# Optimization experiments

Hardware: AMD Instinct MI355X
Metric: run time of the kernel (lower is better)

The kernel has to match this reference:

```python
import jax, jax.numpy as jnp
import numpy as np

# Module constants (from init_kwargs / defaults)
OUT_SIZE = (4, 32, 32)      # (Z, X, Y) grid
REAL_SIZE = (3.0, 25.0, 25.0)
SCALE = 1.4
THRESHOLD = 0.5
D_ELEMS = np.array([0.74 * SCALE, 0.528 * SCALE], dtype=np.float32)  # per-element match/NMS radius (O, H)


def _transform(x):
    """(B, X, Y, Z, 4*E) -> coords (B, E, N, 3), conf (B, E, N); N = Z*X*Y."""
    B, X, Y, Z, L = x.shape
    E = L // 4
    v = x.reshape(B, X, Y, Z, E, 4).transpose(0, 4, 3, 1, 2, 5)   # (B,E,Z,X,Y,4)
    v = v[..., jnp.array([2, 0, 1, 3])]                            # reorder last dim
    Zs, Xs, Ys = OUT_SIZE
    ind = jnp.stack(jnp.meshgrid(jnp.arange(Zs), jnp.arange(Xs), jnp.arange(Ys), indexing='ij'),
                    axis=-1).astype(x.dtype)                       # (Z,X,Y,3) == torch nonzero of ones
    expand = jnp.array([r / o for o, r in zip(OUT_SIZE, REAL_SIZE)], dtype=x.dtype)
    coords = (v[..., :3] + ind) * expand
    conf = v[..., 3]
    N = Zs * Xs * Ys
    return coords.reshape(B, E, N, 3), conf.reshape(B, E, N)


def _sort_by_conf(coords, conf):
    order = jnp.argsort(-conf, axis=-1)
    coords = jnp.take_along_axis(coords, order[..., None], axis=2)
    conf = jnp.take_along_axis(conf, order, axis=-1)
    return coords, conf


def _nms(pts, valid, d):
    """Greedy sequential NMS on one (N,3) point set. Point b is suppressed if any
    still-selected earlier point a<b lies within distance d. Invalid points never suppress."""
    N = pts.shape[0]
    d2 = jnp.sum((pts[:, None, :] - pts[None, :, :]) ** 2, axis=-1)   # (N,N)
    ar = jnp.arange(N)
    M = (d2 < d * d) & valid[:, None] & valid[None, :] & (ar[:, None] < ar[None, :])

    def body(b, sel):
        return sel.at[b].set(~jnp.any(sel & M[:, b]))

    sel = jax.lax.fori_loop(0, N, body, jnp.ones((N,), bool))
    return sel & valid


def _match(P, T, keepP, keepT, d):
    """Greedy row-major bipartite matching: each pred (in order) grabs the first
    still-unmatched target within distance d. Returns (TP, FP, FN) masks."""
    N = P.shape[0]
    d2 = jnp.sum((P[:, None, :] - T[None, :, :]) ** 2, axis=-1)      # (N,N)
    D = (d2 < d * d) & keepP[:, None] & keepT[None, :]

    def body(a, carry):
        selP, selT = carry
        avail = D[a] & ~selT
        has = jnp.any(avail)
        j = jnp.argmax(avail)                    # first available target index
        selT = selT.at[j].set(selT[j] | has)
        selP = selP.at[a].set(has)
        return (selP, selT)

    selP, selT = jax.lax.fori_loop(0, N, body,
                                   (jnp.zeros((N,), bool), jnp.zeros((N,), bool)))
    return selP, keepP & ~selP, keepT & ~selT    # TP, FP, FN masks


def setup_inputs() -> dict:
    key = jax.random.key(0)
    k1, k2 = jax.random.split(key)
    B = 4
    predictions = jax.random.normal(k1, (B, 32, 32, 4, 8), dtype=jnp.float32)
    targets = jax.random.normal(k2, (B, 32, 32, 4, 8), dtype=jnp.float32)
    return {"predictions": predictions, "targets": targets}


def reference(predictions, targets):
    Pc, Pconf = _sort_by_conf(*_transform(predictions))   # (B,E,N,3), (B,E,N)
    Tc, Tconf = _sort_by_conf(*_transform(targets))
    validP = Pconf > THRESHOLD
    validT = Tconf > THRESHOLD
    d = jnp.asarray(D_ELEMS)                               # (E,)

    nms_be = jax.vmap(jax.vmap(_nms, in_axes=(0, 0, 0)), in_axes=(0, 0, None))
    keepP = nms_be(Pc, validP, d)                          # (B,E,N) bool
    keepT = nms_be(Tc, validT, d)

    match_be = jax.vmap(jax.vmap(_match, in_axes=(0, 0, 0, 0, 0)), in_axes=(0, 0, 0, 0, None))
    tp, fp, fn = match_be(Pc, Tc, keepP, keepT, d)         # (B,E,N) bool each

    # sorted real-space points, NMS-kept masks, and TP/FP/FN masks (fixed-shape
    # equivalents of the torch module's filtered P/T/TP/FP/FN lists)
    return Pc, Tc, keepP, keepT, tp, fp, fn
```

## Files before the change

kernel.cpp:

```cpp
#include <hip/hip_runtime.h>
#include <hip/hip_bf16.h>

#pragma clang fp contract(off)

#define NPTS 4096
#define BE   8
#define COORD_SZ (BE * NPTS * 3)
#define MASK_SZ  (BE * NPTS)
#define OFF_PC   0
#define OFF_TC   (COORD_SZ)
#define OFF_KP   (2 * COORD_SZ)
#define OFF_KT   (2 * COORD_SZ + MASK_SZ)
#define OFF_TP   (2 * COORD_SZ + 2 * MASK_SZ)
#define OFF_FP   (2 * COORD_SZ + 3 * MASK_SZ)
#define OFF_FN   (2 * COORD_SZ + 4 * MASK_SZ)

#define VCAP 1664
#define NW   26

#define WS_V_OFF     524288ull
#define WS_KEEP_OFF  524352ull
#define WS_PP_OFF    528448ull
#define WS_PT_OFF    6066240ull
#define WS_NEED      8835136ull

#define NBC 16

typedef unsigned long long u64;

__device__ __forceinline__ float get_dd(int e) {
    const float d0 = (float)(0.74 * 1.4);
    const float d1 = (float)(0.528 * 1.4);
    float d = (e == 0) ? d0 : d1;
    return d * d;
}

__global__ __launch_bounds__(1024)
void sort_kernel(const float* __restrict__ pred,
                 const float* __restrict__ targ,
                 float* __restrict__ out,
                 int* __restrict__ Vcnt) {
    __shared__ u64 bufA[NPTS], bufB[NPTS];
    __shared__ unsigned int hist[1024];
    __shared__ unsigned int offarr[1024];
    __shared__ int wsum[16];
    __shared__ int vtot;
    const int s = blockIdx.x;
    const int arr = s & 1, be = s >> 1;
    const int b = be >> 1, e = be & 1;
    const float* __restrict__ src = arr ? targ : pred;
    const int t = threadIdx.x;
    const int lane = t & 63, wv = t >> 6;

    if (t == 0) vtot = 0;
    for (int n = t; n < NPTS; n += 1024) {
        int z = n >> 10, r = n & 1023, x = r >> 5, y = r & 31;
        int base = (((b * 32 + x) * 32 + y) * 4 + z) * 8 + e * 4;
        float conf = src[base + 3];
        unsigned int bits = __float_as_uint(conf);
        unsigned int u = (bits & 0x80000000u) ? ~bits : (bits | 0x80000000u);
        bufA[n] = ((u64)(~u) << 32) | (unsigned int)n;
    }
    __syncthreads();

    const u64 lmask = (1ull << lane) - 1ull;
    for (int k = 0; k < 8; ++k) {
        u64* cur = (k & 1) ? bufB : bufA;
        u64* nxt = (k & 1) ? bufA : bufB;
        const int shift = 32 + (k << 2);
        hist[t] = 0u;
        __syncthreads();

        u64 item[4]; int dg[4]; int rnk[4];
        #pragma unroll
        for (int m = 0; m < 4; ++m) {
            u64 it = cur[m * 1024 + t];
            int d = (int)((it >> shift) & 15);
            u64 eq = ~0ull;
            #pragma unroll
            for (int bb = 0; bb < 4; ++bb) {
                u64 bal = __ballot((d >> bb) & 1);
                eq &= ((d >> bb) & 1) ? bal : ~bal;
            }
            int r = (int)__popcll(eq & lmask);
            if (r == 0) hist[d * 64 + m * 16 + wv] = (unsigned int)__popcll(eq);
            item[m] = it; dg[m] = d; rnk[m] = r;
        }
        __syncthreads();

        {
            int v = (int)hist[t];
            int inc = v;
            #pragma unroll
            for (int dd = 1; dd < 64; dd <<= 1) {
                int x2 = __shfl_up(inc, dd);
                if (lane >= dd) inc += x2;
            }
            if (lane == 63) wsum[wv] = inc;
            __syncthreads();
            if (t < 16) {
                int wtot = wsum[t]; int iv = wtot;
                #pragma unroll
                for (int dd = 1; dd < 16; dd <<= 1) {
                    int x2 = __shfl_up(iv, dd);
                    if (t >= dd) iv += x2;
                }
                wsum[t] = iv - wtot;
            }
            __syncthreads();
            offarr[t] = (unsigned int)(wsum[wv] + (inc - v));
        }
        __syncthreads();

        #pragma unroll
        for (int m = 0; m < 4; ++m) {
            int pos = (int)offarr[dg[m] * 64 + m * 16 + wv] + rnk[m];
            nxt[pos] = item[m];
        }
        __syncthreads();
    }

    int myv = 0;
    for (int p = t; p < NPTS; p += 1024) {
        u64 key = bufA[p];
        int n = (int)(key & 0xFFFFFFFFull);
        myv += ((unsigned int)(key >> 32) < 0x40FFFFFFu) ? 1 : 0;
        int z = n >> 10, rr = n & 1023, x = rr >> 5, y = rr & 31;
        int base = (((b * 32 + x) * 32 + y) * 4 + z) * 8 + e * 4;
        float r0 = src[base + 0], r1 = src[base + 1], r2 = src[base + 2];
        float c0 = (r2 + (float)z) * 0.75f;
        float c1 = (r0 + (float)x) * 0.78125f;
        float c2 = (r1 + (float)y) * 0.78125f;
        float* dst = out + (size_t)arr * COORD_SZ + ((size_t)be * NPTS + p) * 3;
        dst[0] = c0; dst[1] = c1; dst[2] = c2;
    }
    atomicAdd(&vtot, myv);
    __syncthreads();
    if (t == 0) Vcnt[s] = vtot;
}

__global__ __launch_bounds__(256)
void matrix_kernel(const float* __restrict__ out,
                   const int* __restrict__ Vcnt,
                   u64* __restrict__ ws64) {
    __shared__ float4 tcol[VCAP];
    __shared__ float rowc[64][3];
    const int bx = blockIdx.x;
    const int j = bx / 26, c = bx % 26;
    const int t = threadIdx.x;

    int sRow, sCol, e;
    u64* dstBase;
    if (j < 16) {
        sRow = j; sCol = j; e = (j >> 1) & 1;
        dstBase = ws64 + (WS_PP_OFF / 8) + (size_t)j * VCAP * NW;
    } else {
        int be = j - 16;
        sRow = be * 2 + 0; sCol = be * 2 + 1; e = be & 1;
        dstBase = ws64 + (WS_PT_OFF / 8) + (size_t)be * VCAP * NW;
    }
    int Vr = Vcnt[sRow]; if (Vr > VCAP) Vr = VCAP;
    int Vc = Vcnt[sCol]; if (Vc > VCAP) Vc = VCAP;
    const int rb = c * 64;
    if (rb >= Vr) return;
    const float dd = get_dd(e);

    const float* __restrict__ colc = out + (size_t)(sCol & 1) * COORD_SZ + (size_t)(sCol >> 1) * NPTS * 3;
    const float* __restrict__ rowp = out + (size_t)(sRow & 1) * COORD_SZ + (size_t)(sRow >> 1) * NPTS * 3;

    for (int idx = t; idx < Vc * 3; idx += 256) {
        float v = colc[idx];
        int p = idx / 3, k = idx % 3;
        ((float*)&tcol[p])[k] = v;
    }
    for (int idx = t; idx < 192; idx += 256) {
        int i = idx / 3, k = idx % 3;
        if (rb + i < Vr) rowc[i][k] = rowp[(rb + i) * 3 + k];
    }
    __syncthreads();

    const int NWc = (Vc + 63) >> 6;
    const int wlimit = (j < 16) ? (c + 1) : NWc;
    const int i = t & 63;
    const bool rowOK = (rb + i) < Vr;
    if (rowOK) {
        float ax = rowc[i][0], ay = rowc[i][1], az = rowc[i][2];
        for (int w = t >> 6; w < wlimit; w += 4) {
            int jbase = w << 6;
            int jmax = Vc - jbase; if (jmax > 64) jmax = 64;
            u64 m = 0ull;
            for (int jj = 0; jj < jmax; ++jj) {
                float4 tc = tcol[jbase + jj];
                float dx = ax - tc.x, dy = ay - tc.y, dz = az - tc.z;
                float d2 = dx * dx + dy * dy + dz * dz;
                m |= (d2 < dd) ? (1ull << jj) : 0ull;
            }
            dstBase[(size_t)w * VCAP + (rb + i)] = m;
        }
    }
}

__global__ __launch_bounds__(1024)
void nms_rounds_kernel(float* __restrict__ out,
                       const int* __restrict__ Vcnt,
                       u64* __restrict__ ws64) {
    __shared__ unsigned short nbr[VCAP][NBC];
    __shared__ unsigned short nbrcnt[VCAP];
    __shared__ unsigned char stbuf[VCAP];
    __shared__ int remaining;
    volatile unsigned char* st = stbuf;
    const int s = blockIdx.x;
    const int arr = s & 1, be = s >> 1;
    const int t = threadIdx.x;
    int V = Vcnt[s]; if (V > VCAP) V = VCAP;
    const u64* __restrict__ Mx = ws64 + (WS_PP_OFF / 8) + (size_t)s * VCAP * NW;

    for (int i = t; i < VCAP; i += 1024) stbuf[i] = 0;
    if (t == 0) remaining = V;
    __syncthreads();

    bool und0 = (t < V), und1 = (t + 1024 < V);
    int ndec1 = 0;
    #pragma unroll
    for (int half = 0; half < 2; ++half) {
        const int i = t + half * 1024;
        if (i < V) {
            const int wi = i >> 6;
            int cnt = 0;
            for (int w = 0; w <= wi; ++w) {
                u64 m = Mx[(size_t)w * VCAP + i];
                if (w == wi) m &= (1ull << (i & 63)) - 1ull;
                while (m) {
                    int bb = (int)__builtin_ctzll(m); m &= m - 1ull;
                    if (cnt < NBC) nbr[i][cnt] = (unsigned short)((w << 6) + bb);
                    cnt++;
                }
            }
            nbrcnt[i] = (unsigned short)cnt;
            if (cnt == 0) {
                st[i] = 1;
                if (half == 0) und0 = false; else und1 = false;
                ndec1++;
            }
        }
    }
    if (ndec1) atomicSub(&remaining, ndec1);
    __syncthreads();

    while (remaining > 0) {
        int ndec = 0;
        #pragma unroll
        for (int half = 0; half < 2; ++half) {
            bool& und = (half == 0) ? und0 : und1;
            if (und) {
                const int i = t + half * 1024;
                bool cu = false, ck = false;
                int cnt = nbrcnt[i];
                if (cnt <= NBC) {
                    for (int k = 0; k < cnt; ++k) {
                        int sj = st[nbr[i][k]];
                        ck = ck || (sj == 1);
                        cu = cu || (sj == 0);
                    }
                } else {
                    const int wi = i >> 6;
                    for (int w = 0; w <= wi; ++w) {
                        u64 m = Mx[(size_t)w * VCAP + i];
                        if (w == wi) m &= (1ull << (i & 63)) - 1ull;
                        while (m) {
                            int bb = (int)__builtin_ctzll(m); m &= m - 1ull;
                            int sj = st[(w << 6) + bb];
                            ck = ck || (sj == 1);
                            cu = cu || (sj == 0);
                        }
                    }
                }
                if (ck) {
                    st[i] = 2;
                    und = false; ndec++;
                } else if (!cu) {
                    st[i] = 1;
                    und = false; ndec++;
                }
            }
        }
        if (ndec) atomicSub(&remaining, ndec);
        __syncthreads();
    }

    u64 wlo = __ballot((t < V) && (st[t] == 1));
    u64 whi = __ballot((t + 1024 < V) && (st[t + 1024] == 1));
    u64* kb = ws64 + (WS_KEEP_OFF / 8) + s * 32;
    if ((t & 63) == 0) {
        kb[t >> 6] = wlo;
        kb[16 + (t >> 6)] = whi;
    }
    const size_t kbase = (arr == 0 ? OFF_KP : OFF_KT) + (size_t)be * NPTS;
    for (int p = t; p < NPTS; p += 1024) {
        bool k = (p < V) && (st[p] == 1);
        out[kbase + p] = k ? 1.0f : 0.0f;
    }
}

__global__ __launch_bounds__(1024)
void match_resolve_kernel(float* __restrict__ out,
                          const int* __restrict__ Vcnt,
                          u64* __restrict__ ws64) {
    __shared__ unsigned short cand[VCAP][16];
    __shared__ unsigned short candcnt[VCAP];
    __shared__ unsigned short rowlist[VCAP];
    __shared__ unsigned int colmin[VCAP];
    __shared__ u64 kPw[NW], kTw[NW], availT[NW];
    __shared__ int wp[NW];
    __shared__ int Mcnt, remaining;
    __shared__ unsigned int selP32[128];
    const int be = blockIdx.x;
    const int t = threadIdx.x;
    int Vp = Vcnt[be * 2 + 0]; if (Vp > VCAP) Vp = VCAP;
    int Vt = Vcnt[be * 2 + 1]; if (Vt > VCAP) Vt = VCAP;
    const int NWt = (Vt + 63) >> 6;
    const u64* __restrict__ PT = ws64 + (WS_PT_OFF / 8) + (size_t)be * VCAP * NW;

    if (t < NW) {
        kPw[t] = ws64[(WS_KEEP_OFF / 8) + (be * 2 + 0) * 32 + t];
        kTw[t] = ws64[(WS_KEEP_OFF / 8) + (be * 2 + 1) * 32 + t];
    }
    if (t < 128) selP32[t] = 0u;
    for (int idx = t; idx < VCAP; idx += 1024) colmin[idx] = 0xFFFFFFFFu;
    __syncthreads();

    if (t < 64) {
        int cP = (t < NW) ? __popcll(kPw[t]) : 0;
        int o = cP;
        for (int d = 1; d < 64; d <<= 1) {
            int v = __shfl_up(o, d);
            if (t >= d) o += v;
        }
        if (t < NW) wp[t] = o - cP;
        if (t == NW - 1) Mcnt = o;
    }
    __syncthreads();
    const int M = Mcnt;

    for (int a = t; a < Vp; a += 1024) {
        int w = a >> 6, bb = a & 63;
        u64 word = kPw[w];
        if ((word >> bb) & 1ull) {
            int pos = wp[w] + __popcll(word & ((1ull << bb) - 1ull));
            rowlist[pos] = (unsigned short)a;
        }
    }
    if (t < NW) availT[t] = kTw[t];
    if (t == 0) remaining = M;
    __syncthreads();

    #pragma unroll
    for (int half = 0; half < 2; ++half) {
        int g = t + half * 1024;
        if (g < M) {
            const int a = rowlist[g];
            int cnt = 0;
            for (int w = 0; w < NWt; ++w) {
                u64 m = PT[(size_t)w * VCAP + a] & kTw[w];
                while (m) {
                    int bb = (int)__builtin_ctzll(m); m &= m - 1ull;
                    if (cnt < 16) cand[g][cnt] = (unsigned short)((w << 6) + bb);
                    cnt++;
                }
            }
            candcnt[g] = (unsigned short)(cnt > 16 ? 16 : cnt);
        }
    }
    __syncthreads();

    bool und0 = (t < M);
    bool und1 = (t + 1024 < M);
    int round = 0;

    while (remaining > 0) {
        const unsigned int stampBase = (unsigned int)(4095 - round) << 11;
        int jt0 = -1, jt1 = -1;
        bool dead0 = false, dead1 = false;
        if (und0) {
            const int g = t;
            int cn = candcnt[g];
            for (int k = 0; k < cn; ++k) {
                int j = cand[g][k];
                if ((availT[j >> 6] >> (j & 63)) & 1ull) {
                    if (jt0 < 0) jt0 = j;
                    atomicMin(&colmin[j], stampBase | (unsigned int)g);
                }
            }
            if (jt0 < 0) dead0 = true;
        }
        if (und1) {
            const int g = t + 1024;
            int cn = candcnt[g];
            for (int k = 0; k < cn; ++k) {
                int j = cand[g][k];
                if ((availT[j >> 6] >> (j & 63)) & 1ull) {
                    if (jt1 < 0) jt1 = j;
                    atomicMin(&colmin[j], stampBase | (unsigned int)g);
                }
            }
            if (jt1 < 0) dead1 = true;
        }
        __syncthreads();

        int ndec = 0;
        if (und0) {
            const int g = t;
            if (dead0) { und0 = false; ndec++; }
            else if (colmin[jt0] == (stampBase | (unsigned int)g)) {
                atomicAnd(&availT[jt0 >> 6], ~(1ull << (jt0 & 63)));
                int a = rowlist[g];
                atomicOr(&selP32[a >> 5], 1u << (a & 31));
                und0 = false; ndec++;
            }
        }
        if (und1) {
            const int g = t + 1024;
            if (dead1) { und1 = false; ndec++; }
            else if (colmin[jt1] == (stampBase | (unsigned int)g)) {
                atomicAnd(&availT[jt1 >> 6], ~(1ull << (jt1 & 63)));
                int a = rowlist[g];
                atomicOr(&selP32[a >> 5], 1u << (a & 31));
                und1 = false; ndec++;
            }
        }
        if (ndec) atomicSub(&remaining, ndec);
        ++round;
        __syncthreads();
    }

    for (int n = t; n < NPTS; n += 1024) {
        int w = n >> 6;
        bool kpb = (w < NW) && ((kPw[w] >> (n & 63)) & 1ull);
        bool tpb = (selP32[n >> 5] >> (n & 31)) & 1u;
        bool fnb = (w < NW) && ((availT[w] >> (n & 63)) & 1ull);
        size_t o = (size_t)be * NPTS + n;
        out[OFF_TP + o] = tpb ? 1.0f : 0.0f;
        out[OFF_FP + o] = (kpb && !tpb) ? 1.0f : 0.0f;
        out[OFF_FN + o] = fnb ? 1.0f : 0.0f;
    }
}

#define FVCAP 2048
#define FNWMAX (FVCAP / 64)

__global__ __launch_bounds__(1024)
void sortnms_fallback(const float* __restrict__ pred,
                      const float* __restrict__ targ,
                      float* __restrict__ out,
                      u64* __restrict__ keepbits) {
    __shared__ u64 skey[NPTS];
    __shared__ float px[FVCAP], py[FVCAP], pz[FVCAP];
    __shared__ u64 kept[FNWMAX];
    __shared__ u64 mchunk[64];
    __shared__ int supp[64];
    __shared__ int vcnt;
    const int blk = blockIdx.x;
    const int arr = blk & 1;
    const int be  = blk >> 1;
    const int b = be >> 1, e = be & 1;
    const float* __restrict__ src = arr ? targ : pred;
    const int t = threadIdx.x;
    const float dd = get_dd(e);
    if (t == 0) vcnt = 0;

    for (int n = t; n < NPTS; n += 1024) {
        int z = n >> 10, r = n & 1023, x = r >> 5, y = r & 31;
        int base = (((b * 32 + x) * 32 + y) * 4 + z) * 8 + e * 4;
        float conf = src[base + 3];
        unsigned int bits = __float_as_uint(conf);
        unsigned int u = (bits & 0x80000000u) ? ~bits : (bits | 0x80000000u);
        skey[n] = ((u64)(~u) << 32) | (unsigned int)n;
    }
    __syncthreads();
    for (int k = 2; k <= NPTS; k <<= 1) {
        for (int j = k >> 1; j > 0; j >>= 1) {
            for (int i = t; i < NPTS; i += 1024) {
                int ixj = i ^ j;
                if (ixj > i) {
                    u64 a = skey[i], c = skey[ixj];
                    bool up = ((i & k) == 0);
                    if ((a > c) == up) { skey[i] = c; skey[ixj] = a; }
                }
            }
            __syncthreads();
        }
    }
    int myv = 0;
    for (int p = t; p < NPTS; p += 1024) {
        u64 key = skey[p];
        int n = (int)(key & 0xFFFFFFFFu);
        unsigned int u = ~(unsigned int)(key >> 32);
        myv += (u > 0xBF000000u) ? 1 : 0;
        int z = n >> 10, r = n & 1023, x = r >> 5, y = r & 31;
        int base = (((b * 32 + x) * 32 + y) * 4 + z) * 8 + e * 4;
        float r0 = src[base + 0], r1 = src[base + 1], r2 = src[base + 2];
        float c0 = (r2 + (float)z) * 0.75f;
        float c1 = (r0 + (float)x) * 0.78125f;
        float c2 = (r1 + (float)y) * 0.78125f;
        float* dst = out + (size_t)arr * COORD_SZ + ((size_t)be * NPTS + p) * 3;
        dst[0] = c0; dst[1] = c1; dst[2] = c2;
        if (p < FVCAP) { px[p] = c0; py[p] = c1; pz[p] = c2; }
    }
    atomicAdd(&vcnt, myv);
    if (t < FNWMAX) kept[t] = 0ull;
    __syncthreads();

    int V = vcnt; if (V > FVCAP) V = FVCAP;
    const int nchunks = (V + 63) >> 6;
    for (int c = 0; c < nchunks; ++c) {
        if (t < 64) supp[t] = 0;
        __syncthreads();
        {
            int i = t & 63, s = t >> 6;
            int p = (c << 6) + i;
            if (p < V) {
                float x = px[p], y = py[p], z = pz[p];
                int lim = c << 6;
                bool f = false;
                for (int j = s; j < lim; j += 16) {
                    if ((kept[j >> 6] >> (j & 63)) & 1ull) {
                        float dx = x - px[j], dy = y - py[j], dz = z - pz[j];
                        float d2 = dx * dx + dy * dy + dz * dz;
                        if (d2 < dd) { f = true; break; }
                    }
                }
                if (f) atomicOr(&supp[i], 1);
            }
        }
        __syncthreads();
        if (t < 64) {
            int p = (c << 6) + t;
            u64 m = 0ull;
            if (p < V) {
                float x = px[p], y = py[p], z = pz[p];
                for (int j = 0; j < t; ++j) {
                    int q = (c << 6) + j;
                    float dx = x - px[q], dy = y - py[q], dz = z - pz[q];
                    float d2 = dx * dx + dy * dy + dz * dz;
                    if (d2 < dd) m |= (1ull << j);
                }
            }
            mchunk[t] = m;
        }
        __syncthreads();
        if (t == 0) {
            u64 kw = 0ull;
            int lim = V - (c << 6); if (lim > 64) lim = 64;
            for (int i = 0; i < lim; ++i) {
                bool ki = (supp[i] == 0) && ((mchunk[i] & kw) == 0ull);
                if (ki) kw |= (1ull << i);
            }
            kept[c] = kw;
        }
        __syncthreads();
    }
    const size_t kbase = (arr == 0 ? OFF_KP : OFF_KT) + (size_t)be * NPTS;
    for (int p = t; p < NPTS; p += 1024) {
        bool kb = (p < V) && ((kept[(p >> 6) & (FNWMAX - 1)] >> (p & 63)) & 1ull);
        out[kbase + p] = kb ? 1.0f : 0.0f;
    }
    if (t < 64) keepbits[blk * 64 + t] = (t < FNWMAX) ? kept[t] : 0ull;
}

__global__ __launch_bounds__(1024)
void match_fallback(float* __restrict__ out,
                    const u64* __restrict__ keepbits) {
    __shared__ float tx[FVCAP], ty[FVCAP], tz[FVCAP];
    __shared__ unsigned short tj[FVCAP];
    __shared__ unsigned short aidx[FVCAP];
    __shared__ unsigned short matchPos[FVCAP];
    __shared__ u64 Mask[64][FNWMAX + 1];
    __shared__ u64 kPm[64], kTm[64];
    __shared__ unsigned int selP32[128], selT32[128];
    __shared__ int wpT[64], wpP[64];
    __shared__ int Mcnt2, Kcnt2;
    __shared__ float pcx[64], pcy[64], pcz[64];
    const int be = blockIdx.x;
    const int e = be & 1;
    const int t = threadIdx.x;
    const float dd = get_dd(e);
    const float* __restrict__ Pc = out + OFF_PC + (size_t)be * NPTS * 3;
    const float* __restrict__ Tc = out + OFF_TC + (size_t)be * NPTS * 3;

    if (t < 64) {
        kPm[t] = keepbits[(be * 2 + 0) * 64 + t];
        kTm[t] = keepbits[(be * 2 + 1) * 64 + t];
    }
    if (t < 128) { selP32[t] = 0u; selT32[t] = 0u; }
    __syncthreads();
    if (t < 64) {
        int cT = __popcll(kTm[t]), cP = __popcll(kPm[t]);
        int oT = cT, oP = cP;
        for (int d = 1; d < 64; d <<= 1) {
            int vT = __shfl_up(oT, d);
            int vP = __shfl_up(oP, d);
            if (t >= d) { oT += vT; oP += vP; }
        }
        wpT[t] = oT - cT;
        wpP[t] = oP - cP;
        if (t == 63) {
            Kcnt2 = (oT > FVCAP) ? FVCAP : oT;
            Mcnt2 = (oP > FVCAP) ? FVCAP : oP;
        }
    }
    __syncthreads();
    const int K = Kcnt2, M = Mcnt2;
    for (int n = t; n < NPTS; n += 1024) {
        int w = n >> 6, bb = n & 63;
        u64 bit = 1ull << bb, lowm = bit - 1ull;
        u64 wT = kTm[w], wP = kPm[w];
        if (wT & bit) {
            int pos = wpT[w] + __popcll(wT & lowm);
            if (pos < FVCAP) {
                tx[pos] = Tc[n * 3 + 0];
                ty[pos] = Tc[n * 3 + 1];
                tz[pos] = Tc[n * 3 + 2];
                tj[pos] = (unsigned short)n;
            }
        }
        if (wP & bit) {
            int pos = wpP[w] + __popcll(wP & lowm);
            if (pos < FVCAP) aidx[pos] = (unsigned short)n;
        }
    }
    __syncthreads();

    const int NWc = (K + 63) >> 6;
    const int nchunks = (M + 63) >> 6;
    u64 selTw = 0ull;

    for (int c = 0; c < nchunks; ++c) {
        int cnt = M - (c << 6); if (cnt > 64) cnt = 64;
        if (t < 64 && t < cnt) {
            int a = aidx[(c << 6) + t];
            pcx[t] = Pc[a * 3 + 0];
            pcy[t] = Pc[a * 3 + 1];
            pcz[t] = Pc[a * 3 + 2];
        }
        __syncthreads();
        {
            int i = t & 63, s = t >> 6;
            if (i < cnt) {
                float ax = pcx[i], ay = pcy[i], az = pcz[i];
                for (int w = s; w < NWc; w += 16) {
                    int jmax = K - (w << 6); if (jmax > 64) jmax = 64;
                    int base = w << 6;
                    u64 m = 0ull;
                    for (int jj = 0; jj < jmax; ++jj) {
                        float dx = ax - tx[base + jj];
                        float dy = ay - ty[base + jj];
                        float dz = az - tz[base + jj];
                        float d2 = dx * dx + dy * dy + dz * dz;
                        m |= (d2 < dd) ? (1ull << jj) : 0ull;
                    }
                    Mask[i][w] = m;
                }
            }
        }
        __syncthreads();
        if (t < 64) {
            u64 mnext = (cnt > 0 && t < NWc) ? Mask[0][t] : 0ull;
            for (int i = 0; i < cnt; ++i) {
                u64 mrow = mnext;
                mnext = (i + 1 < cnt && t < NWc) ? Mask[i + 1][t] : 0ull;
                u64 avail = mrow & ~selTw;
                u64 bal = __ballot(avail != 0ull);
                if (bal) {
                    int w0 = (int)__builtin_ctzll(bal);
                    if (t == w0) {
                        int bb = (int)__builtin_ctzll(avail);
                        selTw |= 1ull << bb;
                        matchPos[(c << 6) + i] = (unsigned short)((w0 << 6) + bb);
                    }
                } else if (t == 0) {
                    matchPos[(c << 6) + i] = 0xffffu;
                }
            }
        }
        __syncthreads();
    }
    for (int g = t; g < M; g += 1024) {
        unsigned short pos = matchPos[g];
        if (pos != 0xffffu) {
            int jj = tj[pos];
            int a  = aidx[g];
            atomicOr(&selT32[jj >> 5], 1u << (jj & 31));
            atomicOr(&selP32[a >> 5],  1u << (a & 31));
        }
    }
    __syncthreads();
    for (int n = t; n < NPTS; n += 1024) {
        bool kpb = (kPm[n >> 6] >> (n & 63)) & 1ull;
        bool ktb = (kTm[n >> 6] >> (n & 63)) & 1ull;
        bool tpb = (selP32[n >> 5] >> (n & 31)) & 1u;
        bool stb = (selT32[n >> 5] >> (n & 31)) & 1u;
        size_t o = (size_t)be * NPTS + n;
        out[OFF_TP + o] = tpb ? 1.0f : 0.0f;
        out[OFF_FP + o] = (kpb && !tpb) ? 1.0f : 0.0f;
        out[OFF_FN + o] = (ktb && !stb) ? 1.0f : 0.0f;
    }
}

extern "C" void kernel_launch(void* const* d_in, const int* in_sizes, int n_in,
                              void* d_out, int out_size, void* d_ws, size_t ws_size,
                              hipStream_t stream) {
    const float* pred = (const float*)d_in[0];
    const float* targ = (const float*)d_in[1];
    float* out = (float*)d_out;

    if (ws_size >= WS_NEED) {
        int* Vcnt = (int*)((char*)d_ws + WS_V_OFF);
        u64* ws64 = (u64*)d_ws;

        sort_kernel<<<16, 1024, 0, stream>>>(pred, targ, out, Vcnt);
        matrix_kernel<<<624, 256, 0, stream>>>(out, Vcnt, ws64);
        nms_rounds_kernel<<<16, 1024, 0, stream>>>(out, Vcnt, ws64);
        match_resolve_kernel<<<8, 1024, 0, stream>>>(out, Vcnt, ws64);
    } else {
        u64* keepbits = (u64*)d_ws;
        sortnms_fallback<<<16, 1024, 0, stream>>>(pred, targ, out, keepbits);
        match_fallback<<<8, 1024, 0, stream>>>(out, keepbits);
    }
}
```

Baseline: 149.3 us.

## Fuse four pipeline kernels into one cooperative kernel with grid syncs

Combines the sort, distance-matrix, NMS and matching kernels into a single cooperative launch of 208 blocks of 1024 threads. The stages are separated by grid.sync, and each stage's shared memory overlays the others through a union. The aim is to remove the launch gaps between the four kernels. In exchange, the matrix stage now runs on fewer, larger blocks, most blocks sit idle during the serial stages, and the grid barriers cost time. If the cooperative launch fails, the code falls back to the original four launches.

```diff
diff --git a/kernel.cpp b/kernel.cpp
--- a/kernel.cpp
+++ b/kernel.cpp
@@ -1,7 +1,10 @@
 #include <hip/hip_runtime.h>
 #include <hip/hip_bf16.h>
+#include <hip/hip_cooperative_groups.h>
 
 #pragma clang fp contract(off)
+
+namespace cg = cooperative_groups;
 
 #define NPTS 4096
 #define BE   8
@@ -26,6 +29,8 @@
 
 #define NBC 16
 
+#define FGRID 208
+
 typedef unsigned long long u64;
 
 __device__ __forceinline__ float get_dd(int e) {
@@ -35,40 +40,68 @@
     return d * d;
 }
 
-__global__ __launch_bounds__(1024)
-void sort_kernel(const float* __restrict__ pred,
-                 const float* __restrict__ targ,
-                 float* __restrict__ out,
-                 int* __restrict__ Vcnt) {
-    __shared__ u64 bufA[NPTS], bufB[NPTS];
-    __shared__ unsigned int hist[1024];
-    __shared__ unsigned int offarr[1024];
-    __shared__ int wsum[16];
-    __shared__ int vtot;
-    const int s = blockIdx.x;
+struct SortShared {
+    u64 bufA[NPTS], bufB[NPTS];
+    unsigned int hist[1024];
+    unsigned int offarr[1024];
+    int wsum[16];
+    int vtot;
+};
+struct MatShared {
+    float4 tcol[VCAP];
+    float rowc[64][3];
+};
+struct NmsShared {
+    unsigned short nbr[VCAP][NBC];
+    unsigned short nbrcnt[VCAP];
+    unsigned char stbuf[VCAP];
+    int remaining;
+};
+struct MatchShared {
+    unsigned short cand[VCAP][16];
+    unsigned short candcnt[VCAP];
+    unsigned short rowlist[VCAP];
+    unsigned int colmin[VCAP];
+    u64 kPw[NW], kTw[NW], availT[NW];
+    int wp[NW];
+    int Mcnt, remaining;
+    unsigned int selP32[128];
+};
+union FusedShared {
+    SortShared  srt;
+    MatShared   mat;
+    NmsShared   nms;
+    MatchShared mch;
+};
+
+__device__ void sort_body(SortShared& sm, int s,
+                          const float* __restrict__ pred,
+                          const float* __restrict__ targ,
+                          float* __restrict__ out,
+                          int* __restrict__ Vcnt) {
     const int arr = s & 1, be = s >> 1;
     const int b = be >> 1, e = be & 1;
     const float* __restrict__ src = arr ? targ : pred;
     const int t = threadIdx.x;
     const int lane = t & 63, wv = t >> 6;
 
-    if (t == 0) vtot = 0;
+    if (t == 0) sm.vtot = 0;
     for (int n = t; n < NPTS; n += 1024) {
         int z = n >> 10, r = n & 1023, x = r >> 5, y = r & 31;
         int base = (((b * 32 + x) * 32 + y) * 4 + z) * 8 + e * 4;
         float conf = src[base + 3];
         unsigned int bits = __float_as_uint(conf);
         unsigned int u = (bits & 0x80000000u) ? ~bits : (bits | 0x80000000u);
-        bufA[n] = ((u64)(~u) << 32) | (unsigned int)n;
+        sm.bufA[n] = ((u64)(~u) << 32) | (unsigned int)n;
     }
     __syncthreads();
 
     const u64 lmask = (1ull << lane) - 1ull;
     for (int k = 0; k < 8; ++k) {
-        u64* cur = (k & 1) ? bufB : bufA;
-        u64* nxt = (k & 1) ? bufA : bufB;
+        u64* cur = (k & 1) ? sm.bufB : sm.bufA;
+        u64* nxt = (k & 1) ? sm.bufA : sm.bufB;
         const int shift = 32 + (k << 2);
-        hist[t] = 0u;
+        sm.hist[t] = 0u;
         __syncthreads();
 
         u64 item[4]; int dg[4]; int rnk[4];
@@ -83,38 +116,38 @@
                 eq &= ((d >> bb) & 1) ? bal : ~bal;
             }
             int r = (int)__popcll(eq & lmask);
-            if (r == 0) hist[d * 64 + m * 16 + wv] = (unsigned int)__popcll(eq);
+            if (r == 0) sm.hist[d * 64 + m * 16 + wv] = (unsigned int)__popcll(eq);
             item[m] = it; dg[m] = d; rnk[m] = r;
         }
         __syncthreads();
 
         {
-            int v = (int)hist[t];
+            int v = (int)sm.hist[t];
             int inc = v;
             #pragma unroll
             for (int dd = 1; dd < 64; dd <<= 1) {
                 int x2 = __shfl_up(inc, dd);
                 if (lane >= dd) inc += x2;
             }
-            if (lane == 63) wsum[wv] = inc;
+            if (lane == 63) sm.wsum[wv] = inc;
             __syncthreads();
             if (t < 16) {
-                int wtot = wsum[t]; int iv = wtot;
+                int wtot = sm.wsum[t]; int iv = wtot;
                 #pragma unroll
                 for (int dd = 1; dd < 16; dd <<= 1) {
                     int x2 = __shfl_up(iv, dd);
                     if (t >= dd) iv += x2;
                 }
-                wsum[t] = iv - wtot;
+                sm.wsum[t] = iv - wtot;
             }
             __syncthreads();
-            offarr[t] = (unsigned int)(wsum[wv] + (inc - v));
+            sm.offarr[t] = (unsigned int)(sm.wsum[wv] + (inc - v));
         }
         __syncthreads();
 
         #pragma unroll
         for (int m = 0; m < 4; ++m) {
-            int pos = (int)offarr[dg[m] * 64 + m * 16 + wv] + rnk[m];
+            int pos = (int)sm.offarr[dg[m] * 64 + m * 16 + wv] + rnk[m];
             nxt[pos] = item[m];
         }
         __syncthreads();
@@ -122,7 +155,7 @@
 
     int myv = 0;
     for (int p = t; p < NPTS; p += 1024) {
-        u64 key = bufA[p];
+        u64 key = sm.bufA[p];
         int n = (int)(key & 0xFFFFFFFFull);
         myv += ((unsigned int)(key >> 32) < 0x40FFFFFFu) ? 1 : 0;
         int z = n >> 10, rr = n & 1023, x = rr >> 5, y = rr & 31;
@@ -134,19 +167,16 @@
         float* dst = out + (size_t)arr * COORD_SZ + ((size_t)be * NPTS + p) * 3;
         dst[0] = c0; dst[1] = c1; dst[2] = c2;
     }
-    atomicAdd(&vtot, myv);
-    __syncthreads();
-    if (t == 0) Vcnt[s] = vtot;
-}
-
-__global__ __launch_bounds__(256)
-void matrix_kernel(const float* __restrict__ out,
-                   const int* __restrict__ Vcnt,
-                   u64* __restrict__ ws64) {
-    __shared__ float4 tcol[VCAP];
-    __shared__ float rowc[64][3];
-    const int bx = blockIdx.x;
-    const int j = bx / 26, c = bx % 26;
+    atomicAdd(&sm.vtot, myv);
+    __syncthreads();
+    if (t == 0) Vcnt[s] = sm.vtot;
+}
+
+__device__ void matrix_unit(MatShared& sm, int u, int nthr,
+                            const float* __restrict__ out,
+                            const int* __restrict__ Vcnt,
+                            u64* __restrict__ ws64) {
+    const int j = u / 26, c = u % 26;
     const int t = threadIdx.x;
 
     int sRow, sCol, e;
@@ -168,29 +198,29 @@
     const float* __restrict__ colc = out + (size_t)(sCol & 1) * COORD_SZ + (size_t)(sCol >> 1) * NPTS * 3;
     const float* __restrict__ rowp = out + (size_t)(sRow & 1) * COORD_SZ + (size_t)(sRow >> 1) * NPTS * 3;
 
-    for (int idx = t; idx < Vc * 3; idx += 256) {
+    for (int idx = t; idx < Vc * 3; idx += nthr) {
         float v = colc[idx];
         int p = idx / 3, k = idx % 3;
-        ((float*)&tcol[p])[k] = v;
-    }
-    for (int idx = t; idx < 192; idx += 256) {
+        ((float*)&sm.tcol[p])[k] = v;
+    }
+    for (int idx = t; idx < 192; idx += nthr) {
         int i = idx / 3, k = idx % 3;
-        if (rb + i < Vr) rowc[i][k] = rowp[(rb + i) * 3 + k];
+        if (rb + i < Vr) sm.rowc[i][k] = rowp[(rb + i) * 3 + k];
     }
     __syncthreads();
 
     const int NWc = (Vc + 63) >> 6;
     const int wlimit = (j < 16) ? (c + 1) : NWc;
     const int i = t & 63;
-    const bool rowOK = (rb + i) < Vr;
-    if (rowOK) {
-        float ax = rowc[i][0], ay = rowc[i][1], az = rowc[i][2];
-        for (int w = t >> 6; w < wlimit; w += 4) {
+    const int wstride = nthr >> 6;
+    if ((rb + i) < Vr) {
+        float ax = sm.rowc[i][0], ay = sm.rowc[i][1], az = sm.rowc[i][2];
+        for (int w = t >> 6; w < wlimit; w += wstride) {
             int jbase = w << 6;
             int jmax = Vc - jbase; if (jmax > 64) jmax = 64;
             u64 m = 0ull;
             for (int jj = 0; jj < jmax; ++jj) {
-                float4 tc = tcol[jbase + jj];
+                float4 tc = sm.tcol[jbase + jj];
                 float dx = ax - tc.x, dy = ay - tc.y, dz = az - tc.z;
                 float d2 = dx * dx + dy * dy + dz * dz;
                 m |= (d2 < dd) ? (1ull << jj) : 0ull;
@@ -200,23 +230,18 @@
     }
 }
 
-__global__ __launch_bounds__(1024)
-void nms_rounds_kernel(float* __restrict__ out,
-                       const int* __restrict__ Vcnt,
-                       u64* __restrict__ ws64) {
-    __shared__ unsigned short nbr[VCAP][NBC];
-    __shared__ unsigned short nbrcnt[VCAP];
-    __shared__ unsigned char stbuf[VCAP];
-    __shared__ int remaining;
-    volatile unsigned char* st = stbuf;
-    const int s = blockIdx.x;
+__device__ void nms_body(NmsShared& sm, int s,
+                         float* __restrict__ out,
+                         const int* __restrict__ Vcnt,
+                         u64* __restrict__ ws64) {
+    volatile unsigned char* st = sm.stbuf;
     const int arr = s & 1, be = s >> 1;
     const int t = threadIdx.x;
     int V = Vcnt[s]; if (V > VCAP) V = VCAP;
     const u64* __restrict__ Mx = ws64 + (WS_PP_OFF / 8) + (size_t)s * VCAP * NW;
 
-    for (int i = t; i < VCAP; i += 1024) stbuf[i] = 0;
-    if (t == 0) remaining = V;
+    for (int i = t; i < VCAP; i += 1024) sm.stbuf[i] = 0;
+    if (t == 0) sm.remaining = V;
     __syncthreads();
 
     bool und0 = (t < V), und1 = (t + 1024 < V);
@@ -232,11 +257,11 @@
                 if (w == wi) m &= (1ull << (i & 63)) - 1ull;
                 while (m) {
                     int bb = (int)__builtin_ctzll(m); m &= m - 1ull;
-                    if (cnt < NBC) nbr[i][cnt] = (unsigned short)((w << 6) + bb);
+                    if (cnt < NBC) sm.nbr[i][cnt] = (unsigned short)((w << 6) + bb);
                     cnt++;
                 }
             }
-            nbrcnt[i] = (unsigned short)cnt;
+            sm.nbrcnt[i] = (unsigned short)cnt;
             if (cnt == 0) {
                 st[i] = 1;
                 if (half == 0) und0 = false; else und1 = false;
@@ -244,10 +269,10 @@
             }
         }
     }
-    if (ndec1) atomicSub(&remaining, ndec1);
-    __syncthreads();
-
-    while (remaining > 0) {
+    if (ndec1) atomicSub(&sm.remaining, ndec1);
+    __syncthreads();
+
+    while (sm.remaining > 0) {
         int ndec = 0;
         #pragma unroll
         for (int half = 0; half < 2; ++half) {
@@ -255,10 +280,10 @@
             if (und) {
                 const int i = t + half * 1024;
                 bool cu = false, ck = false;
-                int cnt = nbrcnt[i];
+                int cnt = sm.nbrcnt[i];
                 if (cnt <= NBC) {
                     for (int k = 0; k < cnt; ++k) {
-                        int sj = st[nbr[i][k]];
+                        int sj = st[sm.nbr[i][k]];
                         ck = ck || (sj == 1);
                         cu = cu || (sj == 0);
                     }
@@ -284,7 +309,7 @@
                 }
             }
         }
-        if (ndec) atomicSub(&remaining, ndec);
+        if (ndec) atomicSub(&sm.remaining, ndec);
         __syncthreads();
     }
 
@@ -302,19 +327,10 @@
     }
 }
 
-__global__ __launch_bounds__(1024)
-void match_resolve_kernel(float* __restrict__ out,
-                          const int* __restrict__ Vcnt,
-                          u64* __restrict__ ws64) {
-    __shared__ unsigned short cand[VCAP][16];
-    __shared__ unsigned short candcnt[VCAP];
-    __shared__ unsigned short rowlist[VCAP];
-    __shared__ unsigned int colmin[VCAP];
-    __shared__ u64 kPw[NW], kTw[NW], availT[NW];
-    __shared__ int wp[NW];
-    __shared__ int Mcnt, remaining;
-    __shared__ unsigned int selP32[128];
-    const int be = blockIdx.x;
+__device__ void match_body(MatchShared& sm, int be,
+                           float* __restrict__ out,
+                           const int* __restrict__ Vcnt,
+                           u64* __restrict__ ws64) {
     const int t = threadIdx.x;
     int Vp = Vcnt[be * 2 + 0]; if (Vp > VCAP) Vp = VCAP;
     int Vt = Vcnt[be * 2 + 1]; if (Vt > VCAP) Vt = VCAP;
@@ -322,53 +338,53 @@
     const u64* __restrict__ PT = ws64 + (WS_PT_OFF / 8) + (size_t)be * VCAP * NW;
 
     if (t < NW) {
-        kPw[t] = ws64[(WS_KEEP_OFF / 8) + (be * 2 + 0) * 32 + t];
-        kTw[t] = ws64[(WS_KEEP_OFF / 8) + (be * 2 + 1) * 32 + t];
-    }
-    if (t < 128) selP32[t] = 0u;
-    for (int idx = t; idx < VCAP; idx += 1024) colmin[idx] = 0xFFFFFFFFu;
+        sm.kPw[t] = ws64[(WS_KEEP_OFF / 8) + (be * 2 + 0) * 32 + t];
+        sm.kTw[t] = ws64[(WS_KEEP_OFF / 8) + (be * 2 + 1) * 32 + t];
+    }
+    if (t < 128) sm.selP32[t] = 0u;
+    for (int idx = t; idx < VCAP; idx += 1024) sm.colmin[idx] = 0xFFFFFFFFu;
     __syncthreads();
 
     if (t < 64) {
-        int cP = (t < NW) ? __popcll(kPw[t]) : 0;
+        int cP = (t < NW) ? __popcll(sm.kPw[t]) : 0;
         int o = cP;
         for (int d = 1; d < 64; d <<= 1) {
             int v = __shfl_up(o, d);
             if (t >= d) o += v;
         }
-        if (t < NW) wp[t] = o - cP;
-        if (t == NW - 1) Mcnt = o;
-    }
-    __syncthreads();
-    const int M = Mcnt;
+        if (t < NW) sm.wp[t] = o - cP;
+        if (t == NW - 1) sm.Mcnt = o;
+    }
+    __syncthreads();
+    const int M = sm.Mcnt;
 
     for (int a = t; a < Vp; a += 1024) {
         int w = a >> 6, bb = a & 63;
-        u64 word = kPw[w];
+        u64 word = sm.kPw[w];
         if ((word >> bb) & 1ull) {
-            int pos = wp[w] + __popcll(word & ((1ull << bb) - 1ull));
-            rowlist[pos] = (unsigned short)a;
-        }
-    }
-    if (t < NW) availT[t] = kTw[t];
-    if (t == 0) remaining = M;
+            int pos = sm.wp[w] + __popcll(word & ((1ull << bb) - 1ull));
+            sm.rowlist[pos] = (unsigned short)a;
+        }
+    }
+    if (t < NW) sm.availT[t] = sm.kTw[t];
+    if (t == 0) sm.remaining = M;
     __syncthreads();
 
     #pragma unroll
     for (int half = 0; half < 2; ++half) {
         int g = t + half * 1024;
         if (g < M) {
-            const int a = rowlist[g];
+            const int a = sm.rowlist[g];
             int cnt = 0;
             for (int w = 0; w < NWt; ++w) {
-                u64 m = PT[(size_t)w * VCAP + a] & kTw[w];
+                u64 m = PT[(size_t)w * VCAP + a] & sm.kTw[w];
                 while (m) {
                     int bb = (int)__builtin_ctzll(m); m &= m - 1ull;
-                    if (cnt < 16) cand[g][cnt] = (unsigned short)((w << 6) + bb);
+                    if (cnt < 16) sm.cand[g][cnt] = (unsigned short)((w << 6) + bb);
                     cnt++;
                 }
             }
-            candcnt[g] = (unsigned short)(cnt > 16 ? 16 : cnt);
+            sm.candcnt[g] = (unsigned short)(cnt > 16 ? 16 : cnt);
         }
     }
     __syncthreads();
@@ -377,30 +393,30 @@
     bool und1 = (t + 1024 < M);
     int round = 0;
 
-    while (remaining > 0) {
+    while (sm.remaining > 0) {
         const unsigned int stampBase = (unsigned int)(4095 - round) << 11;
         int jt0 = -1, jt1 = -1;
         bool dead0 = false, dead1 = false;
         if (und0) {
             const int g = t;
-            int cn = candcnt[g];
+            int cn = sm.candcnt[g];
             for (int k = 0; k < cn; ++k) {
-                int j = cand[g][k];
-                if ((availT[j >> 6] >> (j & 63)) & 1ull) {
+                int j = sm.cand[g][k];
+                if ((sm.availT[j >> 6] >> (j & 63)) & 1ull) {
                     if (jt0 < 0) jt0 = j;
-                    atomicMin(&colmin[j], stampBase | (unsigned int)g);
+                    atomicMin(&sm.colmin[j], stampBase | (unsigned int)g);
                 }
             }
             if (jt0 < 0) dead0 = true;
         }
         if (und1) {
             const int g = t + 1024;
-            int cn = candcnt[g];
+            int cn = sm.candcnt[g];
             for (int k = 0; k < cn; ++k) {
-                int j = cand[g][k];
-                if ((availT[j >> 6] >> (j & 63)) & 1ull) {
+                int j = sm.cand[g][k];
+                if ((sm.availT[j >> 6] >> (j & 63)) & 1ull) {
                     if (jt1 < 0) jt1 = j;
-                    atomicMin(&colmin[j], stampBase | (unsigned int)g);
+                    atomicMin(&sm.colmin[j], stampBase | (unsigned int)g);
                 }
             }
             if (jt1 < 0) dead1 = true;
@@ -411,38 +427,94 @@
         if (und0) {
             const int g = t;
             if (dead0) { und0 = false; ndec++; }
-            else if (colmin[jt0] == (stampBase | (unsigned int)g)) {
-                atomicAnd(&availT[jt0 >> 6], ~(1ull << (jt0 & 63)));
-                int a = rowlist[g];
-                atomicOr(&selP32[a >> 5], 1u << (a & 31));
+            else if (sm.colmin[jt0] == (stampBase | (unsigned int)g)) {
+                atomicAnd(&sm.availT[jt0 >> 6], ~(1ull << (jt0 & 63)));
+                int a = sm.rowlist[g];
+                atomicOr(&sm.selP32[a >> 5], 1u << (a & 31));
                 und0 = false; ndec++;
             }
         }
         if (und1) {
             const int g = t + 1024;
             if (dead1) { und1 = false; ndec++; }
-            else if (colmin[jt1] == (stampBase | (unsigned int)g)) {
-                atomicAnd(&availT[jt1 >> 6], ~(1ull << (jt1 & 63)));
-                int a = rowlist[g];
-                atomicOr(&selP32[a >> 5], 1u << (a & 31));
+            else if (sm.colmin[jt1] == (stampBase | (unsigned int)g)) {
+                atomicAnd(&sm.availT[jt1 >> 6], ~(1ull << (jt1 & 63)));
+                int a = sm.rowlist[g];
+                atomicOr(&sm.selP32[a >> 5], 1u << (a & 31));
                 und1 = false; ndec++;
             }
         }
-        if (ndec) atomicSub(&remaining, ndec);
+        if (ndec) atomicSub(&sm.remaining, ndec);
         ++round;
         __syncthreads();
     }
 
     for (int n = t; n < NPTS; n += 1024) {
         int w = n >> 6;
-        bool kpb = (w < NW) && ((kPw[w] >> (n & 63)) & 1ull);
-        bool tpb = (selP32[n >> 5] >> (n & 31)) & 1u;
-        bool fnb = (w < NW) && ((availT[w] >> (n & 63)) & 1ull);
+        bool kpb = (w < NW) && ((sm.kPw[w] >> (n & 63)) & 1ull);
+        bool tpb = (sm.selP32[n >> 5] >> (n & 31)) & 1u;
+        bool fnb = (w < NW) && ((sm.availT[w] >> (n & 63)) & 1ull);
         size_t o = (size_t)be * NPTS + n;
         out[OFF_TP + o] = tpb ? 1.0f : 0.0f;
         out[OFF_FP + o] = (kpb && !tpb) ? 1.0f : 0.0f;
         out[OFF_FN + o] = fnb ? 1.0f : 0.0f;
     }
+}
+
+__global__ __launch_bounds__(1024)
+void fused_all(const float* __restrict__ pred,
+               const float* __restrict__ targ,
+               float* __restrict__ out,
+               int* __restrict__ Vcnt,
+               u64* __restrict__ ws64) {
+    __shared__ FusedShared sh;
+    cg::grid_group grid = cg::this_grid();
+    const int blk = blockIdx.x;
+
+    if (blk < 16) sort_body(sh.srt, blk, pred, targ, out, Vcnt);
+    __threadfence();
+    grid.sync();
+
+    for (int u = blk; u < 624; u += FGRID) {
+        __syncthreads();
+        matrix_unit(sh.mat, u, 1024, out, Vcnt, ws64);
+    }
+    __threadfence();
+    grid.sync();
+
+    if (blk < 16) nms_body(sh.nms, blk, out, Vcnt, ws64);
+    __threadfence();
+    grid.sync();
+
+    if (blk < 8) match_body(sh.mch, blk, out, Vcnt, ws64);
+}
+
+__global__ __launch_bounds__(1024)
+void sort_kernel(const float* __restrict__ pred, const float* __restrict__ targ,
+                 float* __restrict__ out, int* __restrict__ Vcnt) {
+    __shared__ SortShared sm;
+    sort_body(sm, blockIdx.x, pred, targ, out, Vcnt);
+}
+
+__global__ __launch_bounds__(256)
+void matrix_kernel(const float* __restrict__ out, const int* __restrict__ Vcnt,
+                   u64* __restrict__ ws64) {
+    __shared__ MatShared sm;
+    matrix_unit(sm, blockIdx.x, 256, out, Vcnt, ws64);
+}
+
+__global__ __launch_bounds__(1024)
+void nms_rounds_kernel(float* __restrict__ out, const int* __restrict__ Vcnt,
+                       u64* __restrict__ ws64) {
+    __shared__ NmsShared sm;
+    nms_body(sm, blockIdx.x, out, Vcnt, ws64);
+}
+
+__global__ __launch_bounds__(1024)
+void match_resolve_kernel(float* __restrict__ out, const int* __restrict__ Vcnt,
+                          u64* __restrict__ ws64) {
+    __shared__ MatchShared sm;
+    match_body(sm, blockIdx.x, out, Vcnt, ws64);
 }
 
 #define FVCAP 2048
@@ -717,10 +789,18 @@
         int* Vcnt = (int*)((char*)d_ws + WS_V_OFF);
         u64* ws64 = (u64*)d_ws;
 
-        sort_kernel<<<16, 1024, 0, stream>>>(pred, targ, out, Vcnt);
-        matrix_kernel<<<624, 256, 0, stream>>>(out, Vcnt, ws64);
-        nms_rounds_kernel<<<16, 1024, 0, stream>>>(out, Vcnt, ws64);
-        match_resolve_kernel<<<8, 1024, 0, stream>>>(out, Vcnt, ws64);
+        void* args[] = { (void*)&pred, (void*)&targ, (void*)&out,
+                         (void*)&Vcnt, (void*)&ws64 };
+        hipError_t err = hipLaunchCooperativeKernel((const void*)fused_all,
+                                                    dim3(FGRID), dim3(1024),
+                                                    args, 0u, stream);
+        if (err != hipSuccess) {
+            (void)hipGetLastError();
+            sort_kernel<<<16, 1024, 0, stream>>>(pred, targ, out, Vcnt);
+            matrix_kernel<<<624, 256, 0, stream>>>(out, Vcnt, ws64);
+            nms_rounds_kernel<<<16, 1024, 0, stream>>>(out, Vcnt, ws64);
+            match_resolve_kernel<<<8, 1024, 0, stream>>>(out, Vcnt, ws64);
+        }
     } else {
         u64* keepbits = (u64*)d_ws;
         sortnms_fallback<<<16, 1024, 0, stream>>>(pred, targ, out, keepbits);
```

Result: slower. 355.1 us (+137.8%).
